# Kernel optimization log

Hardware: AMD Instinct MI355X
Metric: run time of the kernel (lower is better)

The kernel has to match this reference:

```python
import jax, jax.numpy as jnp
import numpy as np

C = 64   # mamnet_conv_features
NB = 8   # mamnet_res_blocks
KS = 3   # pixelConv ksize
B, H, W = 4, 96, 96

def conv3(x, w, b):
    # 3x3 conv, stride 1, pad 1, NCHW/OIHW
    y = jax.lax.conv_general_dilated(x, w, (1, 1), ((1, 1), (1, 1)),
                                     dimension_numbers=('NCHW', 'OIHW', 'NCHW'))
    return y + b[None, :, None, None]

def pixel_shuffle(x, r):
    b, c, h, w = x.shape
    co = c // (r * r)
    return x.reshape(b, co, r, r, h, w).transpose(0, 1, 4, 2, 5, 3).reshape(b, co, h * r, w * r)

def mam_att(t, high):
    # per-channel spatial variance (unbiased), normalized across channels
    v = jnp.var(t, axis=(2, 3), ddof=1)                 # [B, C]
    m = jnp.mean(v, axis=1, keepdims=True)
    s = jnp.std(v, axis=1, ddof=1, keepdims=True)
    g = 0.5 * jax.nn.sigmoid((v - m) / s)
    if high:
        g = g + 0.5
    return t * g[:, :, None, None]

def pixel_conv(f, img, wk, bk):
    # per-pixel dynamic kernels: gather 3x3 neighborhoods from img, weight by predicted kernels
    pad = (KS - 1) // 2
    ker = conv3(f, wk, bk)                              # [B, 3*KS^2, h, w]
    b, _, h, w = ker.shape
    ker = ker.reshape(b, KS * KS, 3, h, w).transpose(0, 2, 3, 4, 1)  # [B,3,h,w,N]
    xp = jnp.pad(img, ((0, 0), (0, 0), (pad, pad), (pad, pad)))
    # offsets in torch meshgrid 'ij' order: dx outer, dy inner
    patches = jnp.stack([xp[:, :, pad + dx:pad + dx + h, pad + dy:pad + dy + w]
                         for dx in range(-pad, pad + 1)
                         for dy in range(-pad, pad + 1)], axis=-1)    # [B,3,h,w,N]
    return jnp.sum(patches * ker, axis=-1)

def forward(x, w_first, b_first, w_blk1, b_blk1, w_blk2, b_blk2, w_after, b_after,
            w_up1, b_up1, w_up2, b_up2, w_fc1, b_fc1, w_fc2, b_fc2,
            w_kconv, b_kconv, w_final, b_final):
    b, _, h, w = x.shape
    base = jax.image.resize(x, (b, 3, 4 * h, 4 * w), 'bilinear')
    h0 = conv3(x, w_first, b_first)
    t = h0
    for i in range(NB):  # MAMBlocks (fixed small layer count)
        r1 = conv3(jax.nn.relu(conv3(t, w_blk1[i], b_blk1[i])), w_blk2[i], b_blk2[i])
        cd = t.shape[1] // 4  # distilled channels (distill_rate=0.25)
        t = t + jnp.concatenate([mam_att(r1[:, cd:], False), mam_att(r1[:, :cd], True)], axis=1)
    t = h0 + conv3(t, w_after, b_after)
    t = pixel_shuffle(conv3(t, w_up1, b_up1), 2)
    t = pixel_shuffle(conv3(t, w_up2, b_up2), 2)
    t = conv3(t, w_fc1, b_fc1)
    f = conv3(t, w_fc2, b_fc2)
    bil = jax.image.resize(base, (b, 3, 16 * h, 16 * w), 'bilinear')
    out1 = pixel_conv(f, bil, w_kconv, b_kconv)
    out2 = conv3(f, w_final, b_final)
    return base + out1 + out2

def setup_inputs() -> dict:
    key = jax.random.key(0)
    ks = iter(jax.random.split(key, 40))
    def rn(shape, scale=0.05):
        return jax.random.normal(next(ks), shape, jnp.float32) * scale
    return {
        'x': rn((B, 3, H, W), 1.0),
        'w_first': rn((C, 3, 3, 3)), 'b_first': rn((C,), 0.01),
        'w_blk1': rn((NB, C, C, 3, 3)), 'b_blk1': rn((NB, C), 0.01),
        'w_blk2': rn((NB, C, C, 3, 3)), 'b_blk2': rn((NB, C), 0.01),
        'w_after': rn((C, C, 3, 3)), 'b_after': rn((C,), 0.01),
        'w_up1': rn((4 * C, C, 3, 3)), 'b_up1': rn((4 * C,), 0.01),
        'w_up2': rn((4 * C, C, 3, 3)), 'b_up2': rn((4 * C,), 0.01),
        'w_fc1': rn((C, C, 3, 3)), 'b_fc1': rn((C,), 0.01),
        'w_fc2': rn((C, C, 3, 3)), 'b_fc2': rn((C,), 0.01),
        'w_kconv': rn((3 * KS * KS, C, 3, 3)), 'b_kconv': rn((3 * KS * KS,), 0.01),
        'w_final': rn((3, C, 3, 3)), 'b_final': rn((3,), 0.01),
    }

def reference(x, w_first, b_first, w_blk1, b_blk1, w_blk2, b_blk2, w_after, b_after,
              w_up1, b_up1, w_up2, b_up2, w_fc1, b_fc1, w_fc2, b_fc2,
              w_kconv, b_kconv, w_final, b_final):
    return forward(x, w_first, b_first, w_blk1, b_blk1, w_blk2, b_blk2, w_after, b_after,
                   w_up1, b_up1, w_up2, b_up2, w_fc1, b_fc1, w_fc2, b_fc2,
                   w_kconv, b_kconv, w_final, b_final)
```

## Files before the change

### kernel.cpp

```cpp
#include <hip/hip_runtime.h>
#include <hip/hip_bf16.h>
#include <math.h>

#define BB 4
#define CC 64
#define HH 96
#define WW 96

typedef __attribute__((ext_vector_type(8))) short bf16x8;
typedef __attribute__((ext_vector_type(4))) float f32x4;

__device__ __forceinline__ float b2f(unsigned short u) {
    union { unsigned int i; float f; } v; v.i = ((unsigned int)u) << 16; return v.f;
}
__device__ __forceinline__ unsigned short f2b(float f) {
    union { float f; unsigned int i; } v; v.f = f;
    unsigned int r = v.i + 0x7fffu + ((v.i >> 16) & 1u);
    return (unsigned short)(r >> 16);
}

__global__ void k_bilinear4x(const float* __restrict__ in, float* __restrict__ out,
                             int B, int C, int Hin, int Win) {
    int Hout = Hin * 4, Wout = Win * 4;
    long total = (long)B * C * Hout * Wout;
    long idx = blockIdx.x * (long)blockDim.x + threadIdx.x;
    if (idx >= total) return;
    int x = idx % Wout; long r = idx / Wout;
    int y = r % Hout; r /= Hout;
    int c = r % C; int b = (int)(r / C);
    float sy = 0.25f * (y + 0.5f) - 0.5f;
    float sx = 0.25f * (x + 0.5f) - 0.5f;
    int iy0 = (int)floorf(sy); float fy = sy - iy0;
    int ix0 = (int)floorf(sx); float fx = sx - ix0;
    int iy1 = iy0 + 1, ix1 = ix0 + 1;
    iy0 = min(max(iy0, 0), Hin - 1); iy1 = min(max(iy1, 0), Hin - 1);
    ix0 = min(max(ix0, 0), Win - 1); ix1 = min(max(ix1, 0), Win - 1);
    const float* p = in + ((long)(b * C + c) * Hin) * Win;
    float v = (1.f - fy) * ((1.f - fx) * p[iy0 * Win + ix0] + fx * p[iy0 * Win + ix1])
            +        fy  * ((1.f - fx) * p[iy1 * Win + ix0] + fx * p[iy1 * Win + ix1]);
    out[idx] = v;
}

__global__ void k_wprep(const float* __restrict__ src, unsigned short* __restrict__ dst,
                        int coStart, int coEnd, int writeAll, int CoutPad) {
    long tot = 9L * CoutPad * 64;
    long idx = blockIdx.x * 256L + threadIdx.x;
    if (idx >= tot) return;
    const float* s = src + (size_t)blockIdx.y * (coEnd - coStart) * 64 * 9;
    unsigned short* d = dst + (size_t)blockIdx.y * tot;
    int ci = (int)(idx & 63);
    int co = (int)((idx >> 6) % CoutPad);
    int tap = (int)(idx / (64L * CoutPad));
    bool inr = (co >= coStart && co < coEnd);
    if (!inr && !writeAll) return;
    float v = inr ? s[((size_t)(co - coStart) * 64 + ci) * 9 + tap] : 0.f;
    d[((size_t)tap * CoutPad + co) * 64 + ci] = f2b(v);
}

__global__ void k_packbias(const float* __restrict__ bk, const float* __restrict__ bf_,
                           float* __restrict__ dst) {
    int i = threadIdx.x;
    dst[i] = (i < 27) ? bk[i] : (i < 30 ? bf_[i - 27] : 0.f);
}

__global__ void k_first(const float* __restrict__ x, const float* __restrict__ w,
                        const float* __restrict__ bias, unsigned short* __restrict__ h0,
                        unsigned short* __restrict__ t0) {
    __shared__ float lw[64 * 27];
    __shared__ float lb[64];
    for (int i = threadIdx.x; i < 1728; i += 256) lw[i] = w[i];
    if (threadIdx.x < 64) lb[threadIdx.x] = bias[threadIdx.x];
    __syncthreads();
    int pix = blockIdx.x * 256 + threadIdx.x;
    if (pix >= 9216) return;
    int bimg = blockIdx.z;
    int y = pix / 96, x0 = pix - y * 96;
    float nb[27];
#pragma unroll
    for (int ci = 0; ci < 3; ++ci)
#pragma unroll
        for (int ky = 0; ky < 3; ++ky)
#pragma unroll
            for (int kx = 0; kx < 3; ++kx) {
                int py = y + ky - 1, px = x0 + kx - 1;
                nb[ci * 9 + ky * 3 + kx] =
                    ((unsigned)py < 96u && (unsigned)px < 96u)
                        ? x[((size_t)(bimg * 3 + ci) * 9216) + py * 96 + px] : 0.f;
            }
    size_t ro = ((size_t)bimg * 9216 + pix) * 64;
    for (int cg = 0; cg < 8; ++cg) {
        bf16x8 pk;
#pragma unroll
        for (int u = 0; u < 8; ++u) {
            int co = cg * 8 + u;
            float s = lb[co];
#pragma unroll
            for (int t = 0; t < 27; ++t) s += nb[t] * lw[co * 27 + t];
            pk[u] = (short)f2b(s);
        }
        *(bf16x8*)(h0 + ro + cg * 8) = pk;
        *(bf16x8*)(t0 + ro + cg * 8) = pk;
    }
}

template<int MSUB, int NJ>
__global__ __launch_bounds__(256, 2)
void k_mfconv(const unsigned short* __restrict__ in, const unsigned short* __restrict__ wp,
              const float* __restrict__ bias, const unsigned short* __restrict__ addsrc,
              unsigned short* __restrict__ out, float* __restrict__ sums,
              int H, int W, int CoutReal, int CoutPad, int outCs, int TX, int NG,
              long inImgStride, long outImgStride, int flags) {
    __shared__ uint4 ldsWv[9 * NJ * 16 * 8];
    const int tid = threadIdx.x;
    if ((flags & 16) && blockIdx.x == 0 && blockIdx.z == 0) {
        sums[tid] = 0.f; sums[tid + 256] = 0.f;
    }
    int tx, ng;
    {
        int L = blockIdx.x;
        if ((TX & 7) == 0) {
            int xcd = L & 7, loc = L >> 3;
            int t2 = loc / NG;
            tx = xcd * (TX >> 3) + t2;
            ng = loc - t2 * NG;
        } else { tx = L / NG; ng = L - (L / NG) * NG; }
    }
    const int ngBase = ng * (NJ * 16);
    const uint4* wsrc = (const uint4*)wp;
    constexpr int NCH = 9 * NJ * 16 * 8;
#pragma unroll
    for (int i = 0; i < NCH / 256; ++i) {
        int c = tid + i * 256;
        int tap = c / (NJ * 128);
        int rem = c - tap * (NJ * 128);
        int n = rem >> 3, g = c & 7;
        ldsWv[(tap * (NJ * 16) + n) * 8 + (g ^ (n & 7))] =
            wsrc[((size_t)tap * CoutPad + ngBase + n) * 8 + g];
    }
    __syncthreads();
    const bf16x8* ldsF = (const bf16x8*)ldsWv;

    const int lane = tid & 63, wv = tid >> 6;
    const int lr = lane & 15, lk = lane >> 4;
    const unsigned short* inImg = in + (size_t)blockIdx.z * inImgStride;
    unsigned short* outImg = out + (size_t)blockIdx.z * outImgStride;
    const unsigned short* addImg = addsrc ? addsrc + (size_t)blockIdx.z * outImgStride
                                          : (const unsigned short*)0;

    const int mBase = tx * (MSUB * 64) + wv * (MSUB * 16);
    int ys[MSUB], xs[MSUB];
#pragma unroll
    for (int i = 0; i < MSUB; ++i) {
        int m0 = mBase + i * 16;
        ys[i] = m0 / W; xs[i] = m0 - ys[i] * W;
    }

    f32x4 acc[MSUB][NJ];
#pragma unroll
    for (int j = 0; j < NJ; ++j) {
        int n = ngBase + j * 16 + lr;
        float bv = (n < CoutReal) ? bias[n] : 0.f;
#pragma unroll
        for (int i = 0; i < MSUB; ++i) acc[i][j] = (f32x4){bv, bv, bv, bv};
    }

    auto loadA = [&](int g, bf16x8 (&dst)[MSUB]) {
        int tap = g >> 1, kk = g & 1;
        int ky = (tap / 3) - 1, kx = (tap % 3) - 1;
        int koff = kk * 32 + lk * 8;
#pragma unroll
        for (int i2 = 0; i2 < MSUB; ++i2) {
            int py = ys[i2] + ky;
            int px = xs[i2] + lr + kx;
            bf16x8 af = {0, 0, 0, 0, 0, 0, 0, 0};
            if ((unsigned)py < (unsigned)H && (unsigned)px < (unsigned)W)
                af = *(const bf16x8*)(inImg + ((size_t)py * W + px) * 64 + koff);
            dst[i2] = af;
        }
    };

    bf16x8 A0[MSUB], A1[MSUB], A2[MSUB], A3[MSUB];
    loadA(0, A0); loadA(1, A1); loadA(2, A2); loadA(3, A3);

#pragma unroll
    for (int g = 0; g < 18; ++g) {
        const int tap = g >> 1, kk = g & 1;
        bf16x8 bf[NJ];
#pragma unroll
        for (int j = 0; j < NJ; ++j) {
            int n = j * 16 + lr;
            bf[j] = ldsF[(tap * (NJ * 16) + n) * 8 + (((kk << 2) | lk) ^ (n & 7))];
        }
        const int r4 = g & 3;
#pragma unroll
        for (int i2 = 0; i2 < MSUB; ++i2) {
            bf16x8 af = (r4 == 0) ? A0[i2] : (r4 == 1) ? A1[i2]
                       : (r4 == 2) ? A2[i2] : A3[i2];
#pragma unroll
            for (int j = 0; j < NJ; ++j)
                acc[i2][j] = __builtin_amdgcn_mfma_f32_16x16x32_bf16(af, bf[j], acc[i2][j], 0, 0, 0);
        }
        if (g + 4 < 18) {
            if (r4 == 0) loadA(g + 4, A0);
            else if (r4 == 1) loadA(g + 4, A1);
            else if (r4 == 2) loadA(g + 4, A2);
            else loadA(g + 4, A3);
        }
    }

    const bool doRelu = flags & 1, doShuf = flags & 2, doAdd = flags & 4;
#pragma unroll
    for (int i = 0; i < MSUB; ++i) {
        int y = ys[i], xbase = xs[i];
#pragma unroll
        for (int j = 0; j < NJ; ++j) {
            int n = ngBase + j * 16 + lr;
            f32x4 a = acc[i][j];
#pragma unroll
            for (int r = 0; r < 4; ++r) {
                float v = a[r];
                if (doRelu) v = fmaxf(v, 0.f);
                int xcol = xbase + lk * 4 + r;
                if (!doShuf) {
                    size_t o = ((size_t)y * W + xcol) * outCs + n;
                    if (doAdd) v += b2f(addImg[o]);
                    outImg[o] = f2b(v);
                } else {
                    int oc = n >> 2, si = (n >> 1) & 1, sj = n & 1;
                    size_t o = ((size_t)(2 * y + si) * (2 * W) + (2 * xcol + sj)) * 64 + oc;
                    outImg[o] = f2b(v);
                }
            }
        }
    }

    if (flags & 8) {
        __syncthreads();
        float* sred = (float*)ldsWv;
        const int slot = wv * 4 + lk;
#pragma unroll
        for (int j = 0; j < NJ; ++j) {
            float s = 0.f, s2 = 0.f;
#pragma unroll
            for (int i2 = 0; i2 < MSUB; ++i2)
#pragma unroll
                for (int r = 0; r < 4; ++r) {
                    float v = acc[i2][j][r];
                    s += v; s2 += v * v;
                }
            int ch = j * 16 + lr;
            sred[ch * 16 + slot] = s;
            sred[NJ * 256 + ch * 16 + slot] = s2;
        }
        __syncthreads();
        if (tid < NJ * 16) {
            float s = 0.f, s2 = 0.f;
#pragma unroll
            for (int k2 = 0; k2 < 16; ++k2) {
                s += sred[tid * 16 + k2];
                s2 += sred[NJ * 256 + tid * 16 + k2];
            }
            atomicAdd(&sums[blockIdx.z * 128 + ngBase + tid], s);
            atomicAdd(&sums[blockIdx.z * 128 + 64 + ngBase + tid], s2);
        }
    }
}

__global__ void k_apply(unsigned short* __restrict__ t, const unsigned short* __restrict__ r1,
                        const float* __restrict__ sums) {
    __shared__ float sv[64];
    __shared__ float stats[4];
    __shared__ float gg[64];
    int b = blockIdx.x / 288;
    if (threadIdx.x < 64) {
        int c = threadIdx.x;
        const float n = 9216.f;
        float s = sums[b * 128 + c], s2 = sums[b * 128 + 64 + c];
        float mean = s / n;
        sv[c] = (s2 - n * mean * mean) / (n - 1.f);
    }
    __syncthreads();
    if (threadIdx.x == 0) {
        float mA = 0.f; for (int i = 16; i < 64; ++i) mA += sv[i]; mA /= 48.f;
        float sA = 0.f; for (int i = 16; i < 64; ++i) { float d = sv[i] - mA; sA += d * d; }
        sA = sqrtf(sA / 47.f);
        float mB = 0.f; for (int i = 0; i < 16; ++i) mB += sv[i]; mB /= 16.f;
        float sB = 0.f; for (int i = 0; i < 16; ++i) { float d = sv[i] - mB; sB += d * d; }
        sB = sqrtf(sB / 15.f);
        stats[0] = mA; stats[1] = sA; stats[2] = mB; stats[3] = sB;
    }
    __syncthreads();
    if (threadIdx.x < 64) {
        int c = threadIdx.x;
        float g;
        if (c >= 16) {
            float z = (sv[c] - stats[0]) / stats[1];
            g = 0.5f / (1.f + expf(-z));
        } else {
            float z = (sv[c] - stats[2]) / stats[3];
            g = 0.5f / (1.f + expf(-z)) + 0.5f;
        }
        gg[c] = g;
    }
    __syncthreads();
    long tid8 = blockIdx.x * 256L + threadIdx.x;
    int grp = (int)(tid8 & 7);
    long p = tid8 >> 3;
    int cn0 = grp * 8;
    int cs0 = (cn0 < 48) ? cn0 + 16 : cn0 - 48;
    bf16x8 tv = *(bf16x8*)(t + p * 64 + cn0);
    bf16x8 rv = *(const bf16x8*)(r1 + p * 64 + cs0);
    bf16x8 o;
#pragma unroll
    for (int u = 0; u < 8; ++u)
        o[u] = (short)f2b(b2f((unsigned short)tv[u]) + gg[cs0 + u] * b2f((unsigned short)rv[u]));
    *(bf16x8*)(t + p * 64 + cn0) = o;
}

__global__ void k_final(const float* __restrict__ base, const unsigned short* __restrict__ ker,
                        float* __restrict__ out) {
    const int H = 384, W = 384;
    long idx = blockIdx.x * 256L + threadIdx.x;
    if (idx >= (long)H * W) return;
    int x = (int)(idx % W);
    int y = (int)(idx / W);
    const unsigned short* kp = ker + (size_t)idx * 32;

    float o1[3] = {0.f, 0.f, 0.f};
#pragma unroll
    for (int n9 = 0; n9 < 9; ++n9) {
        int dx = n9 / 3 - 1, dy = n9 % 3 - 1;
        int p = y + dx, q = x + dy;
        float bv[3];
        if (p < 0 || q < 0) {
            bv[0] = bv[1] = bv[2] = 0.f;
        } else {
            float syf = 0.25f * p - 0.375f;
            float sxf = 0.25f * q - 0.375f;
            int iy0 = (int)floorf(syf); float fy = syf - iy0;
            int ix0 = (int)floorf(sxf); float fx = sxf - ix0;
            int iy1 = iy0 + 1, ix1 = ix0 + 1;
            iy0 = min(max(iy0, 0), H - 1); iy1 = min(max(iy1, 0), H - 1);
            ix0 = min(max(ix0, 0), W - 1); ix1 = min(max(ix1, 0), W - 1);
#pragma unroll
            for (int c = 0; c < 3; ++c) {
                const float* bp = base + (long)c * H * W;
                bv[c] = (1.f - fy) * ((1.f - fx) * bp[iy0 * W + ix0] + fx * bp[iy0 * W + ix1])
                      +        fy  * ((1.f - fx) * bp[iy1 * W + ix0] + fx * bp[iy1 * W + ix1]);
            }
        }
#pragma unroll
        for (int c = 0; c < 3; ++c)
            o1[c] += bv[c] * b2f(kp[n9 * 3 + c]);
    }

#pragma unroll
    for (int c = 0; c < 3; ++c) {
        long oi = ((long)c * H + y) * W + x;
        out[oi] = base[oi] + b2f(kp[27 + c]) + o1[c];
    }
}

extern "C" void kernel_launch(void* const* d_in, const int* in_sizes, int n_in,
                              void* d_out, int out_size, void* d_ws, size_t ws_size,
                              hipStream_t stream) {
    const float* x       = (const float*)d_in[0];
    const float* w_first = (const float*)d_in[1];
    const float* b_first = (const float*)d_in[2];
    const float* w_blk1  = (const float*)d_in[3];
    const float* b_blk1  = (const float*)d_in[4];
    const float* w_blk2  = (const float*)d_in[5];
    const float* b_blk2  = (const float*)d_in[6];
    const float* w_after = (const float*)d_in[7];
    const float* b_after = (const float*)d_in[8];
    const float* w_up1   = (const float*)d_in[9];
    const float* b_up1   = (const float*)d_in[10];
    const float* w_up2   = (const float*)d_in[11];
    const float* b_up2   = (const float*)d_in[12];
    const float* w_fc1   = (const float*)d_in[13];
    const float* b_fc1   = (const float*)d_in[14];
    const float* w_fc2   = (const float*)d_in[15];
    const float* b_fc2   = (const float*)d_in[16];
    const float* w_kconv = (const float*)d_in[17];
    const float* b_kconv = (const float*)d_in[18];
    const float* w_final = (const float*)d_in[19];
    const float* b_final = (const float*)d_in[20];
    float* outp = (float*)d_out;
    (void)in_sizes; (void)n_in; (void)out_size; (void)ws_size;

    typedef unsigned short u16;
    char* ws = (char*)d_ws;
    size_t off = 0;
    auto alloc = [&](size_t bytes) {
        size_t o = off; off += (bytes + 255) & ~(size_t)255; return o;
    };
    const size_t SMB = (size_t)BB * 9216 * 64 * 2;
    float* base = (float*)(ws + alloc((size_t)BB * 3 * 147456 * 4));
    u16* h0   = (u16*)(ws + alloc(SMB));
    u16* t    = (u16*)(ws + alloc(SMB));
    u16* ta   = (u16*)(ws + alloc(SMB));
    u16* r1   = (u16*)(ws + alloc(SMB));
    float* sums = (float*)(ws + alloc(BB * 128 * 4));
    float* kbias = (float*)(ws + alloc(64 * 4));
    u16* u1   = (u16*)(ws + alloc((size_t)BB * 36864 * 64 * 2));
    u16* bigA = (u16*)(ws + alloc((size_t)147456 * 64 * 2));
    u16* bigB = (u16*)(ws + alloc((size_t)147456 * 64 * 2));
    u16* kerb = (u16*)(ws + alloc((size_t)147456 * 32 * 2));
    u16* wpB1 = (u16*)(ws + alloc((size_t)8 * 9 * 64 * 64 * 2));
    u16* wpB2 = (u16*)(ws + alloc((size_t)8 * 9 * 64 * 64 * 2));
    u16* wpAf = (u16*)(ws + alloc((size_t)9 * 64 * 64 * 2));
    u16* wpU1 = (u16*)(ws + alloc((size_t)9 * 256 * 64 * 2));
    u16* wpU2 = (u16*)(ws + alloc((size_t)9 * 256 * 64 * 2));
    u16* wpF1 = (u16*)(ws + alloc((size_t)9 * 64 * 64 * 2));
    u16* wpF2 = (u16*)(ws + alloc((size_t)9 * 64 * 64 * 2));
    u16* wpKc = (u16*)(ws + alloc((size_t)9 * 32 * 64 * 2));

    k_wprep<<<dim3(144, 8), 256, 0, stream>>>(w_blk1, wpB1, 0, 64, 1, 64);
    k_wprep<<<dim3(144, 8), 256, 0, stream>>>(w_blk2, wpB2, 0, 64, 1, 64);
    k_wprep<<<dim3(144, 1), 256, 0, stream>>>(w_after, wpAf, 0, 64, 1, 64);
    k_wprep<<<dim3(576, 1), 256, 0, stream>>>(w_up1, wpU1, 0, 256, 1, 256);
    k_wprep<<<dim3(576, 1), 256, 0, stream>>>(w_up2, wpU2, 0, 256, 1, 256);
    k_wprep<<<dim3(144, 1), 256, 0, stream>>>(w_fc1, wpF1, 0, 64, 1, 64);
    k_wprep<<<dim3(144, 1), 256, 0, stream>>>(w_fc2, wpF2, 0, 64, 1, 64);
    k_wprep<<<dim3(72, 1), 256, 0, stream>>>(w_kconv, wpKc, 0, 27, 1, 32);
    k_wprep<<<dim3(72, 1), 256, 0, stream>>>(w_final, wpKc, 27, 30, 0, 32);
    k_packbias<<<dim3(1), 64, 0, stream>>>(b_kconv, b_final, kbias);

    k_bilinear4x<<<dim3(6912), 256, 0, stream>>>(x, base, BB, 3, HH, WW);
    k_first<<<dim3(36, 1, BB), 256, 0, stream>>>(x, w_first, b_first, h0, t);

    const long smStride = 9216L * 64;
    for (int i = 0; i < 8; ++i) {
        const u16* wb1 = wpB1 + (size_t)i * 9 * 64 * 64;
        const u16* wb2 = wpB2 + (size_t)i * 9 * 64 * 64;
        k_mfconv<1, 4><<<dim3(144, 1, BB), 256, 0, stream>>>(
            t, wb1, b_blk1 + (size_t)i * 64, nullptr, ta, sums,
            96, 96, 64, 64, 64, 144, 1, smStride, smStride, 1 | 16);
        k_mfconv<1, 4><<<dim3(144, 1, BB), 256, 0, stream>>>(
            ta, wb2, b_blk2 + (size_t)i * 64, nullptr, r1, sums,
            96, 96, 64, 64, 64, 144, 1, smStride, smStride, 8);
        k_apply<<<dim3(1152), 256, 0, stream>>>(t, r1, sums);
    }

    k_mfconv<1, 4><<<dim3(144, 1, BB), 256, 0, stream>>>(
        t, wpAf, b_after, h0, ta, nullptr, 96, 96, 64, 64, 64, 144, 1,
        smStride, smStride, 4);

    k_mfconv<1, 4><<<dim3(576, 1, BB), 256, 0, stream>>>(
        ta, wpU1, b_up1, nullptr, u1, nullptr, 96, 96, 256, 256, 64, 144, 4,
        smStride, 36864L * 64, 2);

    for (int b = 0; b < BB; ++b) {
        const u16* u1b = u1 + (size_t)b * 36864 * 64;
        const float* base_b = base + (size_t)b * 3 * 147456;
        float* out_b = outp + (size_t)b * 3 * 147456;
        k_mfconv<4, 4><<<dim3(576, 1, 1), 256, 0, stream>>>(
            u1b, wpU2, b_up2, nullptr, bigA, nullptr,
            192, 192, 256, 256, 64, 144, 4, 0, 0, 2);
        k_mfconv<4, 4><<<dim3(576, 1, 1), 256, 0, stream>>>(
            bigA, wpF1, b_fc1, nullptr, bigB, nullptr,
            384, 384, 64, 64, 64, 576, 1, 0, 0, 0);
        k_mfconv<4, 4><<<dim3(576, 1, 1), 256, 0, stream>>>(
            bigB, wpF2, b_fc2, nullptr, bigA, nullptr,
            384, 384, 64, 64, 64, 576, 1, 0, 0, 0);
        k_mfconv<4, 2><<<dim3(576, 1, 1), 256, 0, stream>>>(
            bigA, wpKc, kbias, nullptr, kerb, nullptr,
            384, 384, 30, 32, 32, 576, 1, 0, 0, 0);
        k_final<<<dim3(576), 256, 0, stream>>>(base_b, kerb, out_b);
    }
}
```

Measured before the change: 1.145 ms.

## Stage conv weights in two tap phases to shrink LDS and raise occupancy

The 3x3 conv weights are now staged into shared memory in two phases (taps 0-3, then taps 4-8) instead of all nine taps at once, which roughly halves the LDS allocation. Launch bounds go from 2 to 3 blocks per CU. The manual four-deep register prefetch of A fragments is dropped in favour of inline loads just before use, which frees registers. The cost is an extra barrier and weight reload mid-kernel, plus less explicit latency hiding for the global loads, which now relies on higher occupancy and the compiler.

```diff
diff --git a/kernel.cpp b/kernel.cpp
--- a/kernel.cpp
+++ b/kernel.cpp
@@ -103,14 +103,63 @@
     }
 }
 
+template<int TAP0, int NTAP, int MSUB, int NJ>
+__device__ __forceinline__ void conv_phase(const uint4* __restrict__ wsrc,
+                                           uint4* __restrict__ ldsWv,
+                                           const unsigned short* __restrict__ inImg,
+                                           int H, int W, int CoutPad, int ngBase,
+                                           int tid, int lr, int lk,
+                                           const int (&ys)[MSUB], const int (&xs)[MSUB],
+                                           f32x4 (&acc)[MSUB][NJ], bool first) {
+    if (!first) __syncthreads();
+    constexpr int NCH = NTAP * NJ * 128;
+#pragma unroll
+    for (int i = 0; i < NCH / 256; ++i) {
+        int c = tid + i * 256;
+        int lt = c / (NJ * 128);
+        int rem = c - lt * (NJ * 128);
+        int n = rem >> 3, g = c & 7;
+        ldsWv[(lt * (NJ * 16) + n) * 8 + (g ^ (n & 7))] =
+            wsrc[((size_t)(TAP0 + lt) * CoutPad + ngBase + n) * 8 + g];
+    }
+    __syncthreads();
+    const bf16x8* ldsF = (const bf16x8*)ldsWv;
+#pragma unroll
+    for (int lt = 0; lt < NTAP; ++lt) {
+        const int tap = TAP0 + lt;
+        const int ky = tap / 3 - 1, kx = tap % 3 - 1;
+#pragma unroll
+        for (int kk = 0; kk < 2; ++kk) {
+            bf16x8 bf[NJ];
+#pragma unroll
+            for (int j = 0; j < NJ; ++j) {
+                int n = j * 16 + lr;
+                bf[j] = ldsF[(lt * (NJ * 16) + n) * 8 + (((kk << 2) | lk) ^ (n & 7))];
+            }
+            const int koff = kk * 32 + lk * 8;
+#pragma unroll
+            for (int i2 = 0; i2 < MSUB; ++i2) {
+                int py = ys[i2] + ky;
+                int px = xs[i2] + lr + kx;
+                bf16x8 af = {0, 0, 0, 0, 0, 0, 0, 0};
+                if ((unsigned)py < (unsigned)H && (unsigned)px < (unsigned)W)
+                    af = *(const bf16x8*)(inImg + ((size_t)py * W + px) * 64 + koff);
+#pragma unroll
+                for (int j = 0; j < NJ; ++j)
+                    acc[i2][j] = __builtin_amdgcn_mfma_f32_16x16x32_bf16(af, bf[j], acc[i2][j], 0, 0, 0);
+            }
+        }
+    }
+}
+
 template<int MSUB, int NJ>
-__global__ __launch_bounds__(256, 2)
+__global__ __launch_bounds__(256, 3)
 void k_mfconv(const unsigned short* __restrict__ in, const unsigned short* __restrict__ wp,
               const float* __restrict__ bias, const unsigned short* __restrict__ addsrc,
               unsigned short* __restrict__ out, float* __restrict__ sums,
               int H, int W, int CoutReal, int CoutPad, int outCs, int TX, int NG,
               long inImgStride, long outImgStride, int flags) {
-    __shared__ uint4 ldsWv[9 * NJ * 16 * 8];
+    __shared__ uint4 ldsWv[5 * NJ * 16 * 8];
     const int tid = threadIdx.x;
     if ((flags & 16) && blockIdx.x == 0 && blockIdx.z == 0) {
         sums[tid] = 0.f; sums[tid + 256] = 0.f;
@@ -127,18 +176,6 @@
     }
     const int ngBase = ng * (NJ * 16);
     const uint4* wsrc = (const uint4*)wp;
-    constexpr int NCH = 9 * NJ * 16 * 8;
-#pragma unroll
-    for (int i = 0; i < NCH / 256; ++i) {
-        int c = tid + i * 256;
-        int tap = c / (NJ * 128);
-        int rem = c - tap * (NJ * 128);
-        int n = rem >> 3, g = c & 7;
-        ldsWv[(tap * (NJ * 16) + n) * 8 + (g ^ (n & 7))] =
-            wsrc[((size_t)tap * CoutPad + ngBase + n) * 8 + g];
-    }
-    __syncthreads();
-    const bf16x8* ldsF = (const bf16x8*)ldsWv;
 
     const int lane = tid & 63, wv = tid >> 6;
     const int lr = lane & 15, lk = lane >> 4;
@@ -164,49 +201,10 @@
         for (int i = 0; i < MSUB; ++i) acc[i][j] = (f32x4){bv, bv, bv, bv};
     }
 
-    auto loadA = [&](int g, bf16x8 (&dst)[MSUB]) {
-        int tap = g >> 1, kk = g & 1;
-        int ky = (tap / 3) - 1, kx = (tap % 3) - 1;
-        int koff = kk * 32 + lk * 8;
-#pragma unroll
-        for (int i2 = 0; i2 < MSUB; ++i2) {
-            int py = ys[i2] + ky;
-            int px = xs[i2] + lr + kx;
-            bf16x8 af = {0, 0, 0, 0, 0, 0, 0, 0};
-            if ((unsigned)py < (unsigned)H && (unsigned)px < (unsigned)W)
-                af = *(const bf16x8*)(inImg + ((size_t)py * W + px) * 64 + koff);
-            dst[i2] = af;
-        }
-    };
-
-    bf16x8 A0[MSUB], A1[MSUB], A2[MSUB], A3[MSUB];
-    loadA(0, A0); loadA(1, A1); loadA(2, A2); loadA(3, A3);
-
-#pragma unroll
-    for (int g = 0; g < 18; ++g) {
-        const int tap = g >> 1, kk = g & 1;
-        bf16x8 bf[NJ];
-#pragma unroll
-        for (int j = 0; j < NJ; ++j) {
-            int n = j * 16 + lr;
-            bf[j] = ldsF[(tap * (NJ * 16) + n) * 8 + (((kk << 2) | lk) ^ (n & 7))];
-        }
-        const int r4 = g & 3;
-#pragma unroll
-        for (int i2 = 0; i2 < MSUB; ++i2) {
-            bf16x8 af = (r4 == 0) ? A0[i2] : (r4 == 1) ? A1[i2]
-                       : (r4 == 2) ? A2[i2] : A3[i2];
-#pragma unroll
-            for (int j = 0; j < NJ; ++j)
-                acc[i2][j] = __builtin_amdgcn_mfma_f32_16x16x32_bf16(af, bf[j], acc[i2][j], 0, 0, 0);
-        }
-        if (g + 4 < 18) {
-            if (r4 == 0) loadA(g + 4, A0);
-            else if (r4 == 1) loadA(g + 4, A1);
-            else if (r4 == 2) loadA(g + 4, A2);
-            else loadA(g + 4, A3);
-        }
-    }
+    conv_phase<0, 4, MSUB, NJ>(wsrc, ldsWv, inImg, H, W, CoutPad, ngBase,
+                               tid, lr, lk, ys, xs, acc, true);
+    conv_phase<4, 5, MSUB, NJ>(wsrc, ldsWv, inImg, H, W, CoutPad, ngBase,
+                               tid, lr, lk, ys, xs, acc, false);
 
     const bool doRelu = flags & 1, doShuf = flags & 2, doAdd = flags & 4;
 #pragma unroll
```

Result: no change. 1.162 ms (+1.4%).
